# Kernel tuning notes

Measured on AMD Instinct MI355X. Metric: run time of the kernel, lower is better.

Reference implementation:

```python
import jax, jax.numpy as jnp
import numpy as np

N_VARS = 32
D_MODEL = 256
D_MECH = 128
D_NOISE = D_MODEL // 4
N_LAYERS = 3
TEMP = 0.5
BATCH = 512


def gelu(x):
    return jax.nn.gelu(x, approximate=False)  # torch nn.GELU default is exact erf


def setup_inputs() -> dict:
    key = jax.random.key(0)
    ks = jax.random.split(key, 12)
    n, d, m, dn = N_VARS, D_MODEL, D_MECH, D_NOISE
    return {
        "exogenous_noise": jax.random.normal(ks[0], (BATCH, n, dn), dtype=jnp.float32),
        # learned params (edge_logits init randn*0.5 for a nontrivial adjacency)
        "edge_logits": jax.random.normal(ks[1], (n, n), dtype=jnp.float32) * 0.5,
        "var_emb": jax.random.normal(ks[2], (n, d), dtype=jnp.float32) * 0.02,
        # shared parent_aggregate Linear(d, d); weights stored [in, out]
        "pa_W": jax.random.normal(ks[3], (d, d), dtype=jnp.float32) / np.sqrt(d).astype(np.float32),
        "pa_b": jnp.zeros((d,), dtype=jnp.float32),
        # per-variable mechanism MLP weights, stacked on variable axis
        "m_W1": jax.random.normal(ks[4], (n, d, m), dtype=jnp.float32) / np.sqrt(d).astype(np.float32),
        "m_b1": jnp.zeros((n, m), dtype=jnp.float32),
        "m_W2": jax.random.normal(ks[5], (n, m, m), dtype=jnp.float32) / np.sqrt(m).astype(np.float32),
        "m_b2": jnp.zeros((n, m), dtype=jnp.float32),
        "m_W3": jax.random.normal(ks[6], (n, m, d), dtype=jnp.float32) / np.sqrt(m).astype(np.float32),
        "m_b3": jnp.zeros((n, d), dtype=jnp.float32),
        # per-variable noise encoder Linear(dn, d)
        "ne_W": jax.random.normal(ks[7], (n, dn, d), dtype=jnp.float32) / np.sqrt(dn).astype(np.float32),
        "ne_b": jnp.zeros((n, d), dtype=jnp.float32),
    }


def _forward(exogenous_noise, edge_logits, var_emb, pa_W, pa_b,
             m_W1, m_b1, m_W2, m_b2, m_W3, m_b3, ne_W, ne_b):
    n, d = N_VARS, D_MODEL
    batch = exogenous_noise.shape[0]
    # eval-mode adjacency: sigmoid(masked_logits / temp); diagonal masked out
    diag_mask = 1.0 - jnp.eye(n, dtype=edge_logits.dtype)
    adj = jax.nn.sigmoid((edge_logits * diag_mask) / jnp.asarray(TEMP, edge_logits.dtype))
    adj_cols = adj.T                                  # row i = adj[:, i], parents of var i
    noise_t = jnp.transpose(exogenous_noise, (1, 0, 2))  # (n, batch, dn)

    values0 = jnp.zeros((batch, n, d), dtype=exogenous_noise.dtype)
    idx = jnp.arange(n)
    xs = (idx, adj_cols, var_emb, noise_t, m_W1, m_b1, m_W2, m_b2, m_W3, m_b3, ne_W, ne_b)

    def var_step(values, x):
        i, a_col, emb_i, nz, w1, b1, w2, b2, w3, b3, nw, nb = x
        # adjacency-weighted aggregation over ALL current values (sequentially updated)
        pc = jnp.einsum('v,bvd->bd', a_col, values)
        parent_input = gelu((pc + emb_i) @ pa_W + pa_b)
        h = gelu(parent_input @ w1 + b1)
        h = gelu(h @ w2 + b2)
        out = h @ w3 + b3
        out = out + gelu(nz @ nw + nb)               # noise encoder contribution
        values = values.at[:, i].set(out)
        return values, None

    values = values0
    for _ in range(N_LAYERS):
        values, _ = jax.lax.scan(var_step, values, xs)
    return values


def reference(exogenous_noise, edge_logits, var_emb, pa_W, pa_b,
              m_W1, m_b1, m_W2, m_b2, m_W3, m_b3, ne_W, ne_b):
    return _forward(exogenous_noise, edge_logits, var_emb, pa_W, pa_b,
                    m_W1, m_b1, m_W2, m_b2, m_W3, m_b3, ne_W, ne_b)
```

## Files before the change

kernel.cpp:

```cpp
#include <hip/hip_runtime.h>


typedef __bf16 bf16x8 __attribute__((ext_vector_type(8)));
typedef float  f32x4  __attribute__((ext_vector_type(4)));

#define N_VARS 32
#define BTILE 4
#define NBLK 128

#define ELOFF_PA 0
#define ELOFF_W1 65536
#define ELOFF_W2 1114112
#define ELOFF_W3 1638400

#define XSTR 272
#define HSTR 144
#define VSTR 40

__device__ __forceinline__ unsigned short f2b(float f) {
    unsigned u = __float_as_uint(f);
    u += 0x7FFFu + ((u >> 16) & 1u);
    return (unsigned short)(u >> 16);
}

__device__ __forceinline__ float b2f(unsigned short u) {
    return __uint_as_float(((unsigned)u) << 16);
}

__device__ __forceinline__ void bar_lds() {
    asm volatile("s_waitcnt lgkmcnt(0)\n\ts_barrier" ::: "memory");
}

__device__ __forceinline__ float gelu_e(float x) {
    float z  = x * 0.7071067811865476f;
    float az = fabsf(z);
    float t  = __builtin_amdgcn_rcpf(1.0f + 0.47047f * az);
    float p  = t * (0.3480242f + t * (-0.0958798f + t * 0.7478556f));
    float e  = 1.0f - p * __expf(-z * z);
    float er = (z < 0.0f) ? -e : e;
    return 0.5f * x * (1.0f + er);
}

__device__ __forceinline__ float pickq(f32x4 v, int q) {
    float lo = (q & 1) ? v[1] : v[0];
    float hi = (q & 1) ? v[3] : v[2];
    return (q & 2) ? hi : lo;
}
__device__ __forceinline__ float pick4(float x0, float x1, float x2, float x3, int q) {
    float lo = (q & 1) ? x1 : x0;
    float hi = (q & 1) ? x3 : x2;
    return (q & 2) ? hi : lo;
}

__global__ void prep_all(const float* __restrict__ paW, const float* __restrict__ mW1,
                         const float* __restrict__ mW2, const float* __restrict__ mW3,
                         const float* __restrict__ edge, unsigned short* __restrict__ wsb,
                         unsigned short* __restrict__ adjb,
                         const float* __restrict__ noise, const float* __restrict__ neW,
                         const float* __restrict__ neb, float* __restrict__ outp) {
    __shared__ unsigned short tile[32 * 256];
    const int c = blockIdx.x, tid = threadIdx.x;
    if (c < 520) {
        const float* src; unsigned short* dst; int N, KS, ks;
        if (c < 8)        { src = paW;                     dst = wsb + ELOFF_PA;             N = 256; KS = 8; ks = c; }
        else if (c < 264) { int v = (c - 8) >> 3;   ks = (c - 8) & 7;
                            src = mW1 + v * 32768;         dst = wsb + ELOFF_W1 + v * 32768; N = 128; KS = 8; }
        else if (c < 392) { int v = (c - 264) >> 2; ks = (c - 264) & 3;
                            src = mW2 + v * 16384;         dst = wsb + ELOFF_W2 + v * 16384; N = 128; KS = 4; }
        else              { int v = (c - 392) >> 2; ks = (c - 392) & 3;
                            src = mW3 + v * 32768;         dst = wsb + ELOFF_W3 + v * 32768; N = 256; KS = 4; }
        const int kb = ks * 32, nsh = (N == 256) ? 8 : 7;
        for (int t = tid; t < 32 * N; t += 256) {
            int r = t >> nsh, col = t & (N - 1);
            tile[r * N + col] = f2b(src[(kb + r) * N + col]);
        }
        __syncthreads();
        const int nout = (N >> 4) * 64;
        for (int o = tid; o < nout; o += 256) {
            int nt = o >> 6, lane = o & 63;
            int n = nt * 16 + (lane & 15), k0 = (lane >> 4) << 3;
            unsigned e[8];
            #pragma unroll
            for (int j = 0; j < 8; j++) e[j] = tile[(k0 + j) * N + n];
            uint4 pk;
            pk.x = e[0] | (e[1] << 16); pk.y = e[2] | (e[3] << 16);
            pk.z = e[4] | (e[5] << 16); pk.w = e[6] | (e[7] << 16);
            *(uint4*)(dst + ((nt * KS + ks) * 64 + lane) * 8) = pk;
        }
    } else if (c == 520) {
        for (int t = tid; t < 1024; t += 256) {
            int v = t >> 5, ci = t & 31;
            float x = edge[t];
            float m = (v == ci) ? 0.0f : x;
            float a = __builtin_amdgcn_rcpf(1.0f + __expf(-2.0f * m));
            unsigned short hi = f2b(a);
            float rem = a - b2f(hi);
            adjb[ci * 64 + v]      = hi;
            adjb[ci * 64 + 32 + v] = f2b(rem);
        }
    } else {
        int sb = c - 521;
        int i = sb >> 5, g = sb & 31, d = tid;
        float w[64];
        #pragma unroll
        for (int k = 0; k < 64; k++) w[k] = neW[(i * 64 + k) * 256 + d];
        float bias = neb[i * 256 + d];
        for (int bb = 0; bb < 16; bb++) {
            int b = g * 16 + bb;
            const float* nr = noise + (b * 32 + i) * 64;
            float a0 = bias, a1 = 0.f, a2 = 0.f, a3 = 0.f;
            #pragma unroll
            for (int k = 0; k < 16; k++) {
                a0 += nr[4 * k + 0] * w[4 * k + 0];
                a1 += nr[4 * k + 1] * w[4 * k + 1];
                a2 += nr[4 * k + 2] * w[4 * k + 2];
                a3 += nr[4 * k + 3] * w[4 * k + 3];
            }
            outp[(b * 32 + i) * 256 + d] = gelu_e((a0 + a1) + (a2 + a3));
        }
    }
}

#define MFMA16(a, b, c) __builtin_amdgcn_mfma_f32_16x16x32_bf16(a, b, c, 0, 0, 0)

__global__ __launch_bounds__(512) void
scm_main(const float* __restrict__ emb, const float* __restrict__ pab,
         const float* __restrict__ mb1, const float* __restrict__ mb2,
         const float* __restrict__ mb3, const unsigned short* __restrict__ adjb,
         const __bf16* __restrict__ wsbf, float* __restrict__ outp) {
    __shared__ unsigned short valsT[1024 * VSTR];
    __shared__ unsigned short Xs[4 * XSTR];
    __shared__ unsigned short X2[4 * XSTR];
    __shared__ unsigned short Hs1[4 * HSTR];
    __shared__ unsigned short Hs2[4 * HSTR];

    const int tid = threadIdx.x, blk = blockIdx.x;

    {
        uint4 z; z.x = z.y = z.z = z.w = 0;
        for (int k = tid; k < 5120; k += 512) ((uint4*)valsT)[k] = z;
    }

    const int wid = tid >> 6, lane = tid & 63, l15 = lane & 15, q = lane >> 4;
    const int l3 = l15 & 3;
    const int nW = wid * 16 + l15;
    const int n0 = nW, n1 = nW + 128;

    const float pb0 = pab[n0], pb1 = pab[n1];

    bf16x8 paf0[8], paf1[8];
    #pragma unroll
    for (int ks = 0; ks < 8; ks++) {
        paf0[ks] = *(const bf16x8*)(wsbf + ELOFF_PA + ((wid * 8 + ks) * 64 + lane) * 8);
        paf1[ks] = *(const bf16x8*)(wsbf + ELOFF_PA + (((wid + 8) * 8 + ks) * 64 + lane) * 8);
    }

    Xs[q * XSTR + n0] = f2b(emb[n0]);
    Xs[q * XSTR + n1] = f2b(emb[n1]);
    bar_lds();

    for (int s = 0; s < 3 * N_VARS; s++) {
        const int i = s & 31, ni = (s + 1) & 31;
        const bool last = s >= 64;

        float bi1 = mb1[i * 128 + nW];
        float bi2 = mb2[i * 128 + nW];
        float b3a = mb3[i * 256 + n0];
        float b3b = mb3[i * 256 + n1];
        bf16x8 w1f[8];
        #pragma unroll
        for (int ks = 0; ks < 8; ks++)
            w1f[ks] = *(const bf16x8*)(wsbf + ELOFF_W1 + (size_t)i * 32768 +
                                       ((wid * 8 + ks) * 64 + lane) * 8);
        bf16x8 w2f[4], w3f0[4], w3f1[4];
        #pragma unroll
        for (int ks = 0; ks < 4; ks++) {
            w2f[ks]  = *(const bf16x8*)(wsbf + ELOFF_W2 + (size_t)i * 16384 +
                                        ((wid * 4 + ks) * 64 + lane) * 8);
            w3f0[ks] = *(const bf16x8*)(wsbf + ELOFF_W3 + (size_t)i * 32768 +
                                        ((wid * 4 + ks) * 64 + lane) * 8);
            w3f1[ks] = *(const bf16x8*)(wsbf + ELOFF_W3 + (size_t)i * 32768 +
                                        (((wid + 8) * 4 + ks) * 64 + lane) * 8);
        }
        const size_t obq = ((size_t)(blk * BTILE + q) * 32 + i) * 256;
        const float neq0 = outp[obq + n0];
        const float neq1 = outp[obq + n1];
        bf16x8 anh = *(const bf16x8*)(adjb + ni * 64 + q * 8);
        bf16x8 anl = *(const bf16x8*)(adjb + ni * 64 + 32 + q * 8);
        const float ani = b2f(adjb[ni * 64 + i]) + b2f(adjb[ni * 64 + 32 + i]);
        const float e0 = emb[ni * 256 + n0];
        const float e1 = emb[ni * 256 + n1];

        {
            f32x4 a0e = {0, 0, 0, 0}, a0o = {0, 0, 0, 0};
            f32x4 a1e = {0, 0, 0, 0}, a1o = {0, 0, 0, 0};
            #pragma unroll
            for (int ks = 0; ks < 8; ks += 2) {
                bf16x8 af0 = *(const bf16x8*)(Xs + l3 * XSTR + ks * 32 + q * 8);
                bf16x8 af1 = *(const bf16x8*)(Xs + l3 * XSTR + (ks + 1) * 32 + q * 8);
                a0e = MFMA16(af0, paf0[ks], a0e);
                a1e = MFMA16(af0, paf1[ks], a1e);
                a0o = MFMA16(af1, paf0[ks + 1], a0o);
                a1o = MFMA16(af1, paf1[ks + 1], a1o);
            }
            float s0 = pickq(a0e, q) + pickq(a0o, q) + pb0;
            float s1 = pickq(a1e, q) + pickq(a1o, q) + pb1;
            X2[q * XSTR + n0] = f2b(gelu_e(s0));
            X2[q * XSTR + n1] = f2b(gelu_e(s1));
        }
        bar_lds();

        {
            f32x4 aa = {0, 0, 0, 0}, ab = {0, 0, 0, 0};
            f32x4 ac = {0, 0, 0, 0}, ad = {0, 0, 0, 0};
            #pragma unroll
            for (int ks = 0; ks < 8; ks += 4) {
                bf16x8 af0 = *(const bf16x8*)(X2 + l3 * XSTR + ks * 32 + q * 8);
                bf16x8 af1 = *(const bf16x8*)(X2 + l3 * XSTR + (ks + 1) * 32 + q * 8);
                bf16x8 af2 = *(const bf16x8*)(X2 + l3 * XSTR + (ks + 2) * 32 + q * 8);
                bf16x8 af3 = *(const bf16x8*)(X2 + l3 * XSTR + (ks + 3) * 32 + q * 8);
                aa = MFMA16(af0, w1f[ks], aa);
                ab = MFMA16(af1, w1f[ks + 1], ab);
                ac = MFMA16(af2, w1f[ks + 2], ac);
                ad = MFMA16(af3, w1f[ks + 3], ad);
            }
            float sb = (pickq(aa, q) + pickq(ab, q)) +
                       (pickq(ac, q) + pickq(ad, q)) + bi1;
            Hs1[q * HSTR + nW] = f2b(gelu_e(sb));
        }
        bar_lds();

        f32x4 P0[4], P1[4];
        float o0, o1;
        {
            f32x4 ca = {0, 0, 0, 0}, cb = {0, 0, 0, 0};
            #pragma unroll
            for (int ks = 0; ks < 4; ks += 2) {
                bf16x8 af0 = *(const bf16x8*)(Hs1 + l3 * HSTR + ks * 32 + q * 8);
                bf16x8 af1 = *(const bf16x8*)(Hs1 + l3 * HSTR + (ks + 1) * 32 + q * 8);
                ca = MFMA16(af0, w2f[ks], ca);
                cb = MFMA16(af1, w2f[ks + 1], cb);
            }
            #pragma unroll
            for (int t = 0; t < 4; t++) {
                bf16x8 vf0 = *(const bf16x8*)(valsT + (t * 256 + n0) * VSTR + q * 8);
                bf16x8 vf1 = *(const bf16x8*)(valsT + (t * 256 + n1) * VSTR + q * 8);
                f32x4 z = {0, 0, 0, 0};
                P0[t] = MFMA16(anl, vf0, MFMA16(anh, vf0, z));
                P1[t] = MFMA16(anl, vf1, MFMA16(anh, vf1, z));
            }
            o0 = b2f(valsT[(q * 256 + n0) * VSTR + i]);
            o1 = b2f(valsT[(q * 256 + n1) * VSTR + i]);
            float scv = pickq(ca, q) + pickq(cb, q) + bi2;
            Hs2[q * HSTR + nW] = f2b(gelu_e(scv));
        }
        bar_lds();

        {
            f32x4 c0a = {0, 0, 0, 0}, c0b = {0, 0, 0, 0};
            f32x4 c1a = {0, 0, 0, 0}, c1b = {0, 0, 0, 0};
            #pragma unroll
            for (int ks = 0; ks < 4; ks += 2) {
                bf16x8 af0 = *(const bf16x8*)(Hs2 + l3 * HSTR + ks * 32 + q * 8);
                bf16x8 af1 = *(const bf16x8*)(Hs2 + l3 * HSTR + (ks + 1) * 32 + q * 8);
                c0a = MFMA16(af0, w3f0[ks], c0a);
                c1a = MFMA16(af0, w3f1[ks], c1a);
                c0b = MFMA16(af1, w3f0[ks + 1], c0b);
                c1b = MFMA16(af1, w3f1[ks + 1], c1b);
            }
            float v0 = pickq(c0a, q) + pickq(c0b, q) + b3a + neq0;
            float v1 = pickq(c1a, q) + pickq(c1b, q) + b3b + neq1;
            unsigned short ur0 = f2b(v0), ur1 = f2b(v1);
            valsT[(q * 256 + n0) * VSTR + i] = ur0;
            valsT[(q * 256 + n1) * VSTR + i] = ur1;
            if (last) {
                outp[obq + n0] = v0;
                outp[obq + n1] = v1;
            }
            float pc0 = pick4(P0[0][0], P0[1][0], P0[2][0], P0[3][0], q);
            float pc1 = pick4(P1[0][0], P1[1][0], P1[2][0], P1[3][0], q);
            float x0 = pc0 + ani * (b2f(ur0) - o0) + e0;
            float x1 = pc1 + ani * (b2f(ur1) - o1) + e1;
            Xs[q * XSTR + n0] = f2b(x0);
            Xs[q * XSTR + n1] = f2b(x1);
        }
        bar_lds();
    }
}

extern "C" void kernel_launch(void* const* d_in, const int* in_sizes, int n_in,
                              void* d_out, int out_size, void* d_ws, size_t ws_size,
                              hipStream_t stream) {
    (void)in_sizes; (void)n_in; (void)out_size; (void)ws_size;
    const float* noise = (const float*)d_in[0];
    const float* edge  = (const float*)d_in[1];
    const float* emb   = (const float*)d_in[2];
    const float* paW   = (const float*)d_in[3];
    const float* pab   = (const float*)d_in[4];
    const float* mW1   = (const float*)d_in[5];
    const float* mb1   = (const float*)d_in[6];
    const float* mW2   = (const float*)d_in[7];
    const float* mb2   = (const float*)d_in[8];
    const float* mW3   = (const float*)d_in[9];
    const float* mb3   = (const float*)d_in[10];
    const float* neW   = (const float*)d_in[11];
    const float* neb   = (const float*)d_in[12];
    float* outp = (float*)d_out;

    unsigned short* adjb = (unsigned short*)d_ws;
    unsigned short* wsb  = (unsigned short*)((char*)d_ws + 4096);

    prep_all<<<1545, 256, 0, stream>>>(paW, mW1, mW2, mW3, edge, wsb, adjb,
                                       noise, neW, neb, outp);
    scm_main<<<NBLK, 512, 0, stream>>>(emb, pab, mb1, mb2, mb3, adjb,
                                       (const __bf16*)wsb, outp);
}
```

Before: 373.5 us.

## Fold parent-aggregate linear into W3 so values are stored pre-projected

Because the parent aggregation is linear, (sum a_v*values_v + emb) @ paW equals sum a_v*(values_v@paW) + emb@paW. The change precomputes W3@paW, b3@paW, emb@paW+pab and the noise contribution projected through paW. The main loop then keeps pre-projected values and drops the per-step paW matmul and one barrier. The true output is computed with the original W3 only in the last layer. This adds three prep launches and extra bf16 rounding of the folded weights, which may shift accuracy.

```diff
diff --git a/kernel.cpp b/kernel.cpp
--- a/kernel.cpp
+++ b/kernel.cpp
@@ -8,10 +8,16 @@
 #define BTILE 4
 #define NBLK 128
 
-#define ELOFF_PA 0
-#define ELOFF_W1 65536
-#define ELOFF_W2 1114112
-#define ELOFF_W3 1638400
+#define WS_ADJB   0
+#define WS_B3P    4096
+#define WS_EMBP   36864
+#define WS_WSB    69632
+#define ELOFF_PA  0
+#define ELOFF_W1  65536
+#define ELOFF_W2  1114112
+#define ELOFF_W3  1638400
+#define ELOFF_W3P 2686976
+#define WS_NE2    7540736
 
 #define XSTR 272
 #define HSTR 144
@@ -52,23 +58,61 @@
     return (q & 2) ? hi : lo;
 }
 
+#define MFMA16(a, b, c) __builtin_amdgcn_mfma_f32_16x16x32_bf16(a, b, c, 0, 0, 0)
+
+__global__ void prep_lin(const float* __restrict__ paW, const float* __restrict__ mW3,
+                         const float* __restrict__ mb3, const float* __restrict__ emb,
+                         const float* __restrict__ pab,
+                         float* __restrict__ tmpf, float* __restrict__ b3P,
+                         float* __restrict__ embP) {
+    const int b = blockIdx.x, d = threadIdx.x;
+    if (b < 512) {
+        const int v = b >> 4, mg = (b & 15) * 8;
+        const float* w3r = mW3 + (size_t)(v * 128 + mg) * 256;
+        float acc[8];
+        #pragma unroll
+        for (int r = 0; r < 8; r++) acc[r] = 0.f;
+        for (int n = 0; n < 256; n++) {
+            float pa = paW[n * 256 + d];
+            #pragma unroll
+            for (int r = 0; r < 8; r++) acc[r] += w3r[r * 256 + n] * pa;
+        }
+        #pragma unroll
+        for (int r = 0; r < 8; r++)
+            tmpf[(size_t)(v * 128 + mg + r) * 256 + d] = acc[r];
+    } else if (b < 544) {
+        const int v = b - 512;
+        float a = 0.f;
+        for (int n = 0; n < 256; n++) a += mb3[v * 256 + n] * paW[n * 256 + d];
+        b3P[v * 256 + d] = a;
+    } else {
+        const int v = b - 544;
+        float a = pab[d];
+        for (int n = 0; n < 256; n++) a += emb[v * 256 + n] * paW[n * 256 + d];
+        embP[v * 256 + d] = a;
+    }
+}
+
 __global__ void prep_all(const float* __restrict__ paW, const float* __restrict__ mW1,
                          const float* __restrict__ mW2, const float* __restrict__ mW3,
                          const float* __restrict__ edge, unsigned short* __restrict__ wsb,
                          unsigned short* __restrict__ adjb,
                          const float* __restrict__ noise, const float* __restrict__ neW,
-                         const float* __restrict__ neb, float* __restrict__ outp) {
+                         const float* __restrict__ neb, float* __restrict__ outp,
+                         const float* __restrict__ tmpf) {
     __shared__ unsigned short tile[32 * 256];
     const int c = blockIdx.x, tid = threadIdx.x;
-    if (c < 520) {
+    if (c < 648) {
         const float* src; unsigned short* dst; int N, KS, ks;
-        if (c < 8)        { src = paW;                     dst = wsb + ELOFF_PA;             N = 256; KS = 8; ks = c; }
+        if (c < 8)        { src = paW;                     dst = wsb + ELOFF_PA;              N = 256; KS = 8; ks = c; }
         else if (c < 264) { int v = (c - 8) >> 3;   ks = (c - 8) & 7;
-                            src = mW1 + v * 32768;         dst = wsb + ELOFF_W1 + v * 32768; N = 128; KS = 8; }
+                            src = mW1 + v * 32768;         dst = wsb + ELOFF_W1 + v * 32768;  N = 128; KS = 8; }
         else if (c < 392) { int v = (c - 264) >> 2; ks = (c - 264) & 3;
-                            src = mW2 + v * 16384;         dst = wsb + ELOFF_W2 + v * 16384; N = 128; KS = 4; }
-        else              { int v = (c - 392) >> 2; ks = (c - 392) & 3;
-                            src = mW3 + v * 32768;         dst = wsb + ELOFF_W3 + v * 32768; N = 256; KS = 4; }
+                            src = mW2 + v * 16384;         dst = wsb + ELOFF_W2 + v * 16384;  N = 128; KS = 4; }
+        else if (c < 520) { int v = (c - 392) >> 2; ks = (c - 392) & 3;
+                            src = mW3 + v * 32768;         dst = wsb + ELOFF_W3 + v * 32768;  N = 256; KS = 4; }
+        else              { int v = (c - 520) >> 2; ks = (c - 520) & 3;
+                            src = tmpf + v * 32768;        dst = wsb + ELOFF_W3P + v * 32768; N = 256; KS = 4; }
         const int kb = ks * 32, nsh = (N == 256) ? 8 : 7;
         for (int t = tid; t < 32 * N; t += 256) {
             int r = t >> nsh, col = t & (N - 1);
@@ -87,7 +131,7 @@
             pk.z = e[4] | (e[5] << 16); pk.w = e[6] | (e[7] << 16);
             *(uint4*)(dst + ((nt * KS + ks) * 64 + lane) * 8) = pk;
         }
-    } else if (c == 520) {
+    } else if (c == 648) {
         for (int t = tid; t < 1024; t += 256) {
             int v = t >> 5, ci = t & 31;
             float x = edge[t];
@@ -99,7 +143,7 @@
             adjb[ci * 64 + 32 + v] = f2b(rem);
         }
     } else {
-        int sb = c - 521;
+        int sb = c - 649;
         int i = sb >> 5, g = sb & 31, d = tid;
         float w[64];
         #pragma unroll
@@ -121,15 +165,49 @@
     }
 }
 
-#define MFMA16(a, b, c) __builtin_amdgcn_mfma_f32_16x16x32_bf16(a, b, c, 0, 0, 0)
+__global__ void prep_ne2(const float* __restrict__ nep, const __bf16* __restrict__ wsbf,
+                         unsigned short* __restrict__ ne2) {
+    const int tid = threadIdx.x;
+    const int wid = tid >> 6, lane = tid & 63, l15 = lane & 15, q = lane >> 4;
+    const int gt = blockIdx.x * 4 + wid;
+    const int rowbase = gt * 16;
+    bf16x8 afr[8];
+    #pragma unroll
+    for (int ks = 0; ks < 8; ks++) {
+        const float* s = nep + (size_t)(rowbase + l15) * 256 + ks * 32 + q * 8;
+        float4 x0 = *(const float4*)s;
+        float4 x1 = *(const float4*)(s + 4);
+        uint4 pk;
+        pk.x = (unsigned)f2b(x0.x) | ((unsigned)f2b(x0.y) << 16);
+        pk.y = (unsigned)f2b(x0.z) | ((unsigned)f2b(x0.w) << 16);
+        pk.z = (unsigned)f2b(x1.x) | ((unsigned)f2b(x1.y) << 16);
+        pk.w = (unsigned)f2b(x1.z) | ((unsigned)f2b(x1.w) << 16);
+        afr[ks] = __builtin_bit_cast(bf16x8, pk);
+    }
+    #pragma unroll 4
+    for (int nt = 0; nt < 16; nt++) {
+        f32x4 e4 = {0, 0, 0, 0}, o4 = {0, 0, 0, 0};
+        #pragma unroll
+        for (int ks = 0; ks < 8; ks += 2) {
+            bf16x8 b0 = *(const bf16x8*)(wsbf + ELOFF_PA + ((nt * 8 + ks) * 64 + lane) * 8);
+            bf16x8 b1 = *(const bf16x8*)(wsbf + ELOFF_PA + ((nt * 8 + ks + 1) * 64 + lane) * 8);
+            e4 = MFMA16(afr[ks], b0, e4);
+            o4 = MFMA16(afr[ks + 1], b1, o4);
+        }
+        f32x4 a = e4 + o4;
+        #pragma unroll
+        for (int r = 0; r < 4; r++)
+            ne2[(size_t)(rowbase + 4 * q + r) * 256 + nt * 16 + l15] = f2b(a[r]);
+    }
+}
 
 __global__ __launch_bounds__(512) void
-scm_main(const float* __restrict__ emb, const float* __restrict__ pab,
+scm_main(const float* __restrict__ embP, const float* __restrict__ b3Pp,
          const float* __restrict__ mb1, const float* __restrict__ mb2,
          const float* __restrict__ mb3, const unsigned short* __restrict__ adjb,
-         const __bf16* __restrict__ wsbf, float* __restrict__ outp) {
-    __shared__ unsigned short valsT[1024 * VSTR];
-    __shared__ unsigned short Xs[4 * XSTR];
+         const __bf16* __restrict__ wsbf, const unsigned short* __restrict__ ne2,
+         float* __restrict__ outp) {
+    __shared__ unsigned short valsP[1024 * VSTR];
     __shared__ unsigned short X2[4 * XSTR];
     __shared__ unsigned short Hs1[4 * HSTR];
     __shared__ unsigned short Hs2[4 * HSTR];
@@ -138,7 +216,7 @@
 
     {
         uint4 z; z.x = z.y = z.z = z.w = 0;
-        for (int k = tid; k < 5120; k += 512) ((uint4*)valsT)[k] = z;
+        for (int k = tid; k < 5120; k += 512) ((uint4*)valsP)[k] = z;
     }
 
     const int wid = tid >> 6, lane = tid & 63, l15 = lane & 15, q = lane >> 4;
@@ -146,17 +224,8 @@
     const int nW = wid * 16 + l15;
     const int n0 = nW, n1 = nW + 128;
 
-    const float pb0 = pab[n0], pb1 = pab[n1];
-
-    bf16x8 paf0[8], paf1[8];
-    #pragma unroll
-    for (int ks = 0; ks < 8; ks++) {
-        paf0[ks] = *(const bf16x8*)(wsbf + ELOFF_PA + ((wid * 8 + ks) * 64 + lane) * 8);
-        paf1[ks] = *(const bf16x8*)(wsbf + ELOFF_PA + (((wid + 8) * 8 + ks) * 64 + lane) * 8);
-    }
-
-    Xs[q * XSTR + n0] = f2b(emb[n0]);
-    Xs[q * XSTR + n1] = f2b(emb[n1]);
+    X2[q * XSTR + n0] = f2b(gelu_e(embP[n0]));
+    X2[q * XSTR + n1] = f2b(gelu_e(embP[n1]));
     bar_lds();
 
     for (int s = 0; s < 3 * N_VARS; s++) {
@@ -165,50 +234,46 @@
 
         float bi1 = mb1[i * 128 + nW];
         float bi2 = mb2[i * 128 + nW];
-        float b3a = mb3[i * 256 + n0];
-        float b3b = mb3[i * 256 + n1];
         bf16x8 w1f[8];
         #pragma unroll
         for (int ks = 0; ks < 8; ks++)
             w1f[ks] = *(const bf16x8*)(wsbf + ELOFF_W1 + (size_t)i * 32768 +
                                        ((wid * 8 + ks) * 64 + lane) * 8);
-        bf16x8 w2f[4], w3f0[4], w3f1[4];
+        bf16x8 w2f[4], wPf0[4], wPf1[4];
         #pragma unroll
         for (int ks = 0; ks < 4; ks++) {
             w2f[ks]  = *(const bf16x8*)(wsbf + ELOFF_W2 + (size_t)i * 16384 +
                                         ((wid * 4 + ks) * 64 + lane) * 8);
-            w3f0[ks] = *(const bf16x8*)(wsbf + ELOFF_W3 + (size_t)i * 32768 +
+            wPf0[ks] = *(const bf16x8*)(wsbf + ELOFF_W3P + (size_t)i * 32768 +
                                         ((wid * 4 + ks) * 64 + lane) * 8);
-            w3f1[ks] = *(const bf16x8*)(wsbf + ELOFF_W3 + (size_t)i * 32768 +
+            wPf1[ks] = *(const bf16x8*)(wsbf + ELOFF_W3P + (size_t)i * 32768 +
                                         (((wid + 8) * 4 + ks) * 64 + lane) * 8);
         }
-        const size_t obq = ((size_t)(blk * BTILE + q) * 32 + i) * 256;
-        const float neq0 = outp[obq + n0];
-        const float neq1 = outp[obq + n1];
+        const size_t nrow = ((size_t)(blk * BTILE + q) * 32 + i) * 256;
+        const float ne2_0 = b2f(ne2[nrow + n0]);
+        const float ne2_1 = b2f(ne2[nrow + n1]);
+        const float b3P0 = b3Pp[i * 256 + n0];
+        const float b3P1 = b3Pp[i * 256 + n1];
+        const float eP0 = embP[ni * 256 + n0];
+        const float eP1 = embP[ni * 256 + n1];
         bf16x8 anh = *(const bf16x8*)(adjb + ni * 64 + q * 8);
         bf16x8 anl = *(const bf16x8*)(adjb + ni * 64 + 32 + q * 8);
         const float ani = b2f(adjb[ni * 64 + i]) + b2f(adjb[ni * 64 + 32 + i]);
-        const float e0 = emb[ni * 256 + n0];
-        const float e1 = emb[ni * 256 + n1];
-
-        {
-            f32x4 a0e = {0, 0, 0, 0}, a0o = {0, 0, 0, 0};
-            f32x4 a1e = {0, 0, 0, 0}, a1o = {0, 0, 0, 0};
-            #pragma unroll
-            for (int ks = 0; ks < 8; ks += 2) {
-                bf16x8 af0 = *(const bf16x8*)(Xs + l3 * XSTR + ks * 32 + q * 8);
-                bf16x8 af1 = *(const bf16x8*)(Xs + l3 * XSTR + (ks + 1) * 32 + q * 8);
-                a0e = MFMA16(af0, paf0[ks], a0e);
-                a1e = MFMA16(af0, paf1[ks], a1e);
-                a0o = MFMA16(af1, paf0[ks + 1], a0o);
-                a1o = MFMA16(af1, paf1[ks + 1], a1o);
-            }
-            float s0 = pickq(a0e, q) + pickq(a0o, q) + pb0;
-            float s1 = pickq(a1e, q) + pickq(a1o, q) + pb1;
-            X2[q * XSTR + n0] = f2b(gelu_e(s0));
-            X2[q * XSTR + n1] = f2b(gelu_e(s1));
-        }
-        bar_lds();
+        bf16x8 w3f0[4], w3f1[4];
+        float b3a = 0.f, b3b = 0.f, neq0 = 0.f, neq1 = 0.f;
+        if (last) {
+            #pragma unroll
+            for (int ks = 0; ks < 4; ks++) {
+                w3f0[ks] = *(const bf16x8*)(wsbf + ELOFF_W3 + (size_t)i * 32768 +
+                                            ((wid * 4 + ks) * 64 + lane) * 8);
+                w3f1[ks] = *(const bf16x8*)(wsbf + ELOFF_W3 + (size_t)i * 32768 +
+                                            (((wid + 8) * 4 + ks) * 64 + lane) * 8);
+            }
+            b3a = mb3[i * 256 + n0];
+            b3b = mb3[i * 256 + n1];
+            neq0 = outp[nrow + n0];
+            neq1 = outp[nrow + n1];
+        }
 
         {
             f32x4 aa = {0, 0, 0, 0}, ab = {0, 0, 0, 0};
@@ -231,7 +296,7 @@
         bar_lds();
 
         f32x4 P0[4], P1[4];
-        float o0, o1;
+        float oP0, oP1;
         {
             f32x4 ca = {0, 0, 0, 0}, cb = {0, 0, 0, 0};
             #pragma unroll
@@ -243,14 +308,14 @@
             }
             #pragma unroll
             for (int t = 0; t < 4; t++) {
-                bf16x8 vf0 = *(const bf16x8*)(valsT + (t * 256 + n0) * VSTR + q * 8);
-                bf16x8 vf1 = *(const bf16x8*)(valsT + (t * 256 + n1) * VSTR + q * 8);
+                bf16x8 vf0 = *(const bf16x8*)(valsP + (t * 256 + n0) * VSTR + q * 8);
+                bf16x8 vf1 = *(const bf16x8*)(valsP + (t * 256 + n1) * VSTR + q * 8);
                 f32x4 z = {0, 0, 0, 0};
                 P0[t] = MFMA16(anl, vf0, MFMA16(anh, vf0, z));
                 P1[t] = MFMA16(anl, vf1, MFMA16(anh, vf1, z));
             }
-            o0 = b2f(valsT[(q * 256 + n0) * VSTR + i]);
-            o1 = b2f(valsT[(q * 256 + n1) * VSTR + i]);
+            oP0 = b2f(valsP[(q * 256 + n0) * VSTR + i]);
+            oP1 = b2f(valsP[(q * 256 + n1) * VSTR + i]);
             float scv = pickq(ca, q) + pickq(cb, q) + bi2;
             Hs2[q * HSTR + nW] = f2b(gelu_e(scv));
         }
@@ -263,26 +328,37 @@
             for (int ks = 0; ks < 4; ks += 2) {
                 bf16x8 af0 = *(const bf16x8*)(Hs2 + l3 * HSTR + ks * 32 + q * 8);
                 bf16x8 af1 = *(const bf16x8*)(Hs2 + l3 * HSTR + (ks + 1) * 32 + q * 8);
-                c0a = MFMA16(af0, w3f0[ks], c0a);
-                c1a = MFMA16(af0, w3f1[ks], c1a);
-                c0b = MFMA16(af1, w3f0[ks + 1], c0b);
-                c1b = MFMA16(af1, w3f1[ks + 1], c1b);
-            }
-            float v0 = pickq(c0a, q) + pickq(c0b, q) + b3a + neq0;
-            float v1 = pickq(c1a, q) + pickq(c1b, q) + b3b + neq1;
-            unsigned short ur0 = f2b(v0), ur1 = f2b(v1);
-            valsT[(q * 256 + n0) * VSTR + i] = ur0;
-            valsT[(q * 256 + n1) * VSTR + i] = ur1;
-            if (last) {
-                outp[obq + n0] = v0;
-                outp[obq + n1] = v1;
-            }
+                c0a = MFMA16(af0, wPf0[ks], c0a);
+                c1a = MFMA16(af0, wPf1[ks], c1a);
+                c0b = MFMA16(af1, wPf0[ks + 1], c0b);
+                c1b = MFMA16(af1, wPf1[ks + 1], c1b);
+            }
+            float nP0 = pickq(c0a, q) + pickq(c0b, q) + b3P0 + ne2_0;
+            float nP1 = pickq(c1a, q) + pickq(c1b, q) + b3P1 + ne2_1;
+            unsigned short ur0 = f2b(nP0), ur1 = f2b(nP1);
+            valsP[(q * 256 + n0) * VSTR + i] = ur0;
+            valsP[(q * 256 + n1) * VSTR + i] = ur1;
             float pc0 = pick4(P0[0][0], P0[1][0], P0[2][0], P0[3][0], q);
             float pc1 = pick4(P1[0][0], P1[1][0], P1[2][0], P1[3][0], q);
-            float x0 = pc0 + ani * (b2f(ur0) - o0) + e0;
-            float x1 = pc1 + ani * (b2f(ur1) - o1) + e1;
-            Xs[q * XSTR + n0] = f2b(x0);
-            Xs[q * XSTR + n1] = f2b(x1);
+            float x0 = pc0 + ani * (b2f(ur0) - oP0) + eP0;
+            float x1 = pc1 + ani * (b2f(ur1) - oP1) + eP1;
+            X2[q * XSTR + n0] = f2b(gelu_e(x0));
+            X2[q * XSTR + n1] = f2b(gelu_e(x1));
+            if (last) {
+                f32x4 d0a = {0, 0, 0, 0}, d0b = {0, 0, 0, 0};
+                f32x4 d1a = {0, 0, 0, 0}, d1b = {0, 0, 0, 0};
+                #pragma unroll
+                for (int ks = 0; ks < 4; ks += 2) {
+                    bf16x8 af0 = *(const bf16x8*)(Hs2 + l3 * HSTR + ks * 32 + q * 8);
+                    bf16x8 af1 = *(const bf16x8*)(Hs2 + l3 * HSTR + (ks + 1) * 32 + q * 8);
+                    d0a = MFMA16(af0, w3f0[ks], d0a);
+                    d1a = MFMA16(af0, w3f1[ks], d1a);
+                    d0b = MFMA16(af1, w3f0[ks + 1], d0b);
+                    d1b = MFMA16(af1, w3f1[ks + 1], d1b);
+                }
+                outp[nrow + n0] = pickq(d0a, q) + pickq(d0b, q) + b3a + neq0;
+                outp[nrow + n1] = pickq(d1a, q) + pickq(d1b, q) + b3b + neq1;
+            }
         }
         bar_lds();
     }
@@ -307,11 +383,17 @@
     const float* neb   = (const float*)d_in[12];
     float* outp = (float*)d_out;
 
-    unsigned short* adjb = (unsigned short*)d_ws;
-    unsigned short* wsb  = (unsigned short*)((char*)d_ws + 4096);
-
-    prep_all<<<1545, 256, 0, stream>>>(paW, mW1, mW2, mW3, edge, wsb, adjb,
-                                       noise, neW, neb, outp);
-    scm_main<<<NBLK, 512, 0, stream>>>(emb, pab, mb1, mb2, mb3, adjb,
-                                       (const __bf16*)wsb, outp);
-}
+    unsigned short* adjb = (unsigned short*)((char*)d_ws + WS_ADJB);
+    float* b3P  = (float*)((char*)d_ws + WS_B3P);
+    float* embP = (float*)((char*)d_ws + WS_EMBP);
+    unsigned short* wsb  = (unsigned short*)((char*)d_ws + WS_WSB);
+    float* tmpf = (float*)((char*)d_ws + WS_NE2);
+    unsigned short* ne2u = (unsigned short*)((char*)d_ws + WS_NE2);
+
+    prep_lin<<<576, 256, 0, stream>>>(paW, mW3, mb3, emb, pab, tmpf, b3P, embP);
+    prep_all<<<1673, 256, 0, stream>>>(paW, mW1, mW2, mW3, edge, wsb, adjb,
+                                       noise, neW, neb, outp, tmpf);
+    prep_ne2<<<256, 256, 0, stream>>>(outp, (const __bf16*)wsb, ne2u);
+    scm_main<<<NBLK, 512, 0, stream>>>(embP, b3P, mb1, mb2, mb3, adjb,
+                                       (const __bf16*)wsb, ne2u, outp);
+}
```

Result: slower. 424.1 us (+13.6%).
